# Kernel optimization log

Hardware: AMD Instinct MI355X
Metric: run time of the kernel (lower is better)

The kernel has to match this reference:

```python
import jax, jax.numpy as jnp
import numpy as np

N = 100000  # nodes
E = 1600000  # edges


def gcn_layer(x, src, dst, W, b, n):
    # GCNConv with normalize=True: add self-loops, symmetric deg normalization,
    # linear transform, scatter-add aggregate, add bias, then ReLU (applied by caller).
    loop = jnp.arange(n, dtype=src.dtype)
    s = jnp.concatenate([src, loop])
    d = jnp.concatenate([dst, loop])
    w = jnp.ones(s.shape[0], x.dtype)
    deg = jax.ops.segment_sum(w, d, num_segments=n)
    dis = jnp.where(deg > 0, jax.lax.rsqrt(deg), 0.0)
    norm = dis[s] * w * dis[d]            # [E+N]
    h = x @ W                              # [N, out]
    msg = h[s] * norm[:, None]             # [E+N, out] gather + scale
    out = jax.ops.segment_sum(msg, d, num_segments=n) + b
    return out


def setup_inputs() -> dict:
    key = jax.random.key(0)
    ks = jax.random.split(key, 8)
    d = 128
    sc = 0.05
    return {
        "x": jax.random.normal(ks[0], (N, d), jnp.float32),
        "edge_index": jax.random.randint(ks[1], (2, E), 0, N, jnp.int32),
        "W1": jax.random.normal(ks[2], (d, d), jnp.float32) * sc,
        "b1": jnp.zeros((d,), jnp.float32),
        "W2": jax.random.normal(ks[3], (d, d), jnp.float32) * sc,
        "b2": jnp.zeros((d,), jnp.float32),
        "W3": jax.random.normal(ks[4], (d, d), jnp.float32) * sc,
        "b3": jnp.zeros((d,), jnp.float32),
        "Wm1": jax.random.normal(ks[5], (d, d), jnp.float32) * sc,
        "bm1": jnp.zeros((d,), jnp.float32),
        "Wm2": jax.random.normal(ks[6], (d, 40), jnp.float32) * sc,
        "bm2": jnp.zeros((40,), jnp.float32),
    }


def reference(x, edge_index, W1, b1, W2, b2, W3, b3, Wm1, bm1, Wm2, bm2):
    src, dst = edge_index[0], edge_index[1]
    n = x.shape[0]
    h = x
    for W, b in ((W1, b1), (W2, b2), (W3, b3)):
        h = jax.nn.relu(gcn_layer(h, src, dst, W, b, n))  # emb_normlize=False
    emb = h  # concate=False -> last layer output
    # MLP head: Linear -> ELU -> (dropout p=0, eval) -> Linear -> softmax
    m = jax.nn.elu(emb @ Wm1 + bm1)
    logits = m @ Wm2 + bm2
    probs = jax.nn.softmax(logits, axis=-1)
    return (logits, probs, emb)
```

## Files before the change

### kernel.cpp

```cpp
#include <hip/hip_runtime.h>
#include <math.h>

#define D 128
#define BINW 256
#define MAXBIN 400
#define ACHUNK 4096
#define BCAP 6144
#define SBCAP 8192

typedef __attribute__((ext_vector_type(4))) float floatx4;
typedef __attribute__((ext_vector_type(8))) _Float16 half8;
typedef __attribute__((ext_vector_type(4))) _Float16 half4;


__global__ __launch_bounds__(256) void k_zero(int* __restrict__ p, int n) {
  int i = blockIdx.x * 256 + threadIdx.x;
  if (i < n) p[i] = 0;
}

__global__ __launch_bounds__(256) void k_passA(const int* __restrict__ src,
                                               const int* __restrict__ dst,
                                               int* __restrict__ gbincur,
                                               unsigned* __restrict__ staging,
                                               int E, int nbin) {
  __shared__ int hist[MAXBIN];
  __shared__ int lstart[MAXBIN];
  __shared__ int lcur[MAXBIN];
  __shared__ int runbase[MAXBIN];
  __shared__ int runcnt[MAXBIN];
  __shared__ int sd[256];
  __shared__ unsigned sbuf[ACHUNK];

  int tid = threadIdx.x;
  int e0 = blockIdx.x * ACHUNK;
  int e1 = e0 + ACHUNK < E ? e0 + ACHUNK : E;

  for (int i = tid; i < nbin; i += 256) hist[i] = 0;
  __syncthreads();
  for (int e = e0 + tid; e < e1; e += 256) atomicAdd(&hist[dst[e] >> 8], 1);
  __syncthreads();

  int a = (2 * tid < nbin) ? hist[2 * tid] : 0;
  int b = (2 * tid + 1 < nbin) ? hist[2 * tid + 1] : 0;
  int s = a + b;
  sd[tid] = s;
  __syncthreads();
  for (int off = 1; off < 256; off <<= 1) {
    int t = (tid >= off) ? sd[tid - off] : 0;
    __syncthreads();
    sd[tid] += t;
    __syncthreads();
  }
  int excl = sd[tid] - s;
  if (2 * tid < nbin) lstart[2 * tid] = excl;
  if (2 * tid + 1 < nbin) lstart[2 * tid + 1] = excl + a;
  __syncthreads();

  for (int bx = tid; bx < nbin; bx += 256) {
    int cb = hist[bx];
    int old = cb ? atomicAdd(&gbincur[bx], cb) : 0;
    int lim = SBCAP - old;
    runcnt[bx] = cb < lim ? cb : (lim > 0 ? lim : 0);
    runbase[bx] = bx * SBCAP + old;
    lcur[bx] = lstart[bx];
  }
  __syncthreads();

  for (int e = e0 + tid; e < e1; e += 256) {
    int dd = dst[e];
    int bb = dd >> 8;
    int p = atomicAdd(&lcur[bb], 1);
    sbuf[p] = ((unsigned)src[e] << 8) | (unsigned)(dd & 255);
  }
  __syncthreads();

  int wv = tid >> 6, ln = tid & 63;
  for (int bx = wv; bx < nbin; bx += 4) {
    int cb = runcnt[bx], ls = lstart[bx], rb = runbase[bx];
    for (int i = ln; i < cb; i += 64) staging[rb + i] = sbuf[ls + i];
  }
}

__global__ __launch_bounds__(256) void k_nodehist(const unsigned* __restrict__ staging,
                                                  const int* __restrict__ gbincur,
                                                  int* __restrict__ counts, int N) {
  __shared__ int cnt[BINW];
  int b = blockIdx.x;
  cnt[threadIdx.x] = 0;
  __syncthreads();
  int len = gbincur[b];
  if (len > SBCAP) len = SBCAP;
  int s = b * SBCAP;
  for (int i = (int)threadIdx.x; i < len; i += 256)
    atomicAdd(&cnt[staging[s + i] & 255], 1);
  __syncthreads();
  int node = b * BINW + (int)threadIdx.x;
  if (node < N) counts[node] = cnt[threadIdx.x];
}

__global__ __launch_bounds__(256) void k_scan1(const int* __restrict__ in,
                                               int* __restrict__ out,
                                               int* __restrict__ bsum, int n) {
  __shared__ int sd[256];
  int tid = threadIdx.x;
  int base = blockIdx.x * 1024 + tid * 4;
  int v0 = 0, v1 = 0, v2 = 0, v3 = 0;
  if (base + 3 < n) {
    int4 t = *(const int4*)(in + base);
    v0 = t.x; v1 = t.y; v2 = t.z; v3 = t.w;
  } else {
    if (base     < n) v0 = in[base];
    if (base + 1 < n) v1 = in[base + 1];
    if (base + 2 < n) v2 = in[base + 2];
    if (base + 3 < n) v3 = in[base + 3];
  }
  int s = v0 + v1 + v2 + v3;
  sd[tid] = s;
  __syncthreads();
  for (int off = 1; off < 256; off <<= 1) {
    int t = (tid >= off) ? sd[tid - off] : 0;
    __syncthreads();
    sd[tid] += t;
    __syncthreads();
  }
  int incl = sd[tid];
  int excl = incl - s;
  if (tid == 255) bsum[blockIdx.x] = incl;
  int r = excl;
  if (base     < n) out[base]     = r; r += v0;
  if (base + 1 < n) out[base + 1] = r; r += v1;
  if (base + 2 < n) out[base + 2] = r; r += v2;
  if (base + 3 < n) out[base + 3] = r;
}

__global__ __launch_bounds__(256) void k_scan2(int* __restrict__ bsum, int nb) {
  __shared__ int sd[256];
  int tid = threadIdx.x;
  int v = (tid < nb) ? bsum[tid] : 0;
  sd[tid] = v;
  __syncthreads();
  for (int off = 1; off < 256; off <<= 1) {
    int t = (tid >= off) ? sd[tid - off] : 0;
    __syncthreads();
    sd[tid] += t;
    __syncthreads();
  }
  int excl = sd[tid] - v;
  if (tid < nb) bsum[tid] = excl;
}

__global__ __launch_bounds__(256) void k_finish(int* __restrict__ rowptr,
                                                float* __restrict__ dis,
                                                const int* __restrict__ counts,
                                                const int* __restrict__ bsum, int n) {
  int i = blockIdx.x * 256 + threadIdx.x;
  if (i < n) {
    int r = rowptr[i] + bsum[i >> 10];
    rowptr[i] = r;
    dis[i] = rsqrtf((float)(counts[i] + 1));
  }
}

__global__ __launch_bounds__(256) void k_passB2(const unsigned* __restrict__ staging,
                                                const int* __restrict__ gbincur,
                                                const int* __restrict__ rowptr,
                                                const float* __restrict__ dis,
                                                int2* __restrict__ cpack, int N) {
  __shared__ int lcnt[BINW];
  __shared__ int2 obuf[BCAP];
  int b = blockIdx.x, tid = threadIdx.x;
  int node0 = b * BINW;
  int len = gbincur[b];
  if (len > SBCAP) len = SBCAP;
  int s = b * SBCAP;
  int base = rowptr[node0];
  int node = node0 + tid;
  lcnt[tid] = (node < N) ? (rowptr[node] - base) : 0;
  __syncthreads();
  if (len <= BCAP) {
    for (int i = tid; i < len; i += 256) {
      unsigned pk = staging[s + i];
      int sn = (int)(pk >> 8), dl = (int)(pk & 255u);
      float nw = dis[sn] * dis[node0 + dl];
      int p = atomicAdd(&lcnt[dl], 1);
      obuf[p] = make_int2(sn, __float_as_int(nw));
    }
    __syncthreads();
    for (int i = tid; i < len; i += 256) cpack[base + i] = obuf[i];
  } else {
    for (int i = tid; i < len; i += 256) {
      unsigned pk = staging[s + i];
      int sn = (int)(pk >> 8), dl = (int)(pk & 255u);
      float nw = dis[sn] * dis[node0 + dl];
      int p = atomicAdd(&lcnt[dl], 1);
      cpack[base + p] = make_int2(sn, __float_as_int(nw));
    }
  }
}


__global__ __launch_bounds__(256) void k_prep(const float* __restrict__ W1,
                                              const float* __restrict__ W2,
                                              const float* __restrict__ W3,
                                              const float* __restrict__ Wm1,
                                              const float* __restrict__ Wm2,
                                              _Float16* __restrict__ wsplit,
                                              _Float16* __restrict__ w2h,
                                              _Float16* __restrict__ w2l) {
  int idx = blockIdx.x * 256 + threadIdx.x;
  if (idx < 65536) {
    int w = idx >> 14;
    int rem = idx & 16383;
    int c = rem >> 7, k = rem & 127;
    const float* Ws = (w == 0) ? W1 : (w == 1) ? W2 : (w == 2) ? W3 : Wm1;
    float v = Ws[k * D + c];
    _Float16 hi = (_Float16)v;
    _Float16 lo = (_Float16)(v - (float)hi);
    wsplit[(size_t)w * 32768 + rem] = hi;
    wsplit[(size_t)w * 32768 + 16384 + rem] = lo;
  } else if (idx < 65536 + 6144) {
    int i2 = idx - 65536;
    int c = i2 >> 7, k = i2 & 127;
    float v = (c < 40) ? Wm2[k * 40 + c] : 0.f;
    _Float16 hi = (_Float16)v;
    _Float16 lo = (_Float16)(v - (float)hi);
    w2h[i2] = hi;
    w2l[i2] = lo;
  }
}


__device__ __forceinline__ float elu1(float x) {
  return x > 0.f ? x : (expf(x) - 1.f);
}

template <int AMODE>
__device__ __forceinline__ void loadA(const float* __restrict__ Xf,
                                      const _Float16* __restrict__ Xh,
                                      long rc, int q, half8* ah, half8* al) {
  if (AMODE == 2) {
#pragma unroll
    for (int ks = 0; ks < 4; ks++)
      ah[ks] = *(const half8*)(Xh + rc * D + ks * 32 + q * 8);
  } else {
    const floatx4* x0 = (const floatx4*)(Xf + rc * D);
#pragma unroll
    for (int ks = 0; ks < 4; ks++) {
      floatx4 a0 = x0[ks * 8 + q * 2], a0b = x0[ks * 8 + q * 2 + 1];
#pragma unroll
      for (int j = 0; j < 4; j++) {
        float v = a0[j]; _Float16 h = (_Float16)v;
        ah[ks][j] = h; al[ks][j] = (_Float16)(v - (float)h);
        v = a0b[j]; h = (_Float16)v;
        ah[ks][4 + j] = h; al[ks][4 + j] = (_Float16)(v - (float)h);
      }
    }
  }
}

template <int AMODE, int ACT>
__global__ __launch_bounds__(256, 2) void k_gemm(const float* __restrict__ Xf,
                                                 const _Float16* __restrict__ Xh,
                                                 const _Float16* __restrict__ Whf,
                                                 const _Float16* __restrict__ Wlf,
                                                 const float* __restrict__ bias,
                                                 _Float16* __restrict__ Yh,
                                                 int n, int ntiles) {
  int tid = threadIdx.x;
  int wave = tid >> 6, lane = tid & 63;
  int q = lane >> 4, r = lane & 15;
  int colhalf = wave & 1;
  int stream = wave >> 1;

  half8 wf[4][4][2];
#pragma unroll
  for (int ct = 0; ct < 4; ct++) {
    int c = colhalf * 64 + ct * 16 + r;
#pragma unroll
    for (int ks = 0; ks < 4; ks++) {
      wf[ct][ks][0] = *(const half8*)(Whf + c * D + ks * 32 + q * 8);
      wf[ct][ks][1] = *(const half8*)(Wlf + c * D + ks * 32 + q * 8);
    }
  }

  int tstride = gridDim.x * 2;
  int t = blockIdx.x * 2 + stream;
  if (t >= ntiles) return;

  half8 ah[4], al[4], ahn[4], aln[4];
  {
    long row = (long)t * 16 + r;
    long rc = row < n ? row : (n - 1);
    loadA<AMODE>(Xf, Xh, rc, q, ah, al);
  }

  while (t < ntiles) {
    int tn = t + tstride;
    if (tn < ntiles) {
      long rown = (long)tn * 16 + r;
      long rcn = rown < n ? rown : (n - 1);
      loadA<AMODE>(Xf, Xh, rcn, q, ahn, aln);
    }

    floatx4 acc[4];
#pragma unroll
    for (int ct = 0; ct < 4; ct++) acc[ct] = (floatx4){0.f, 0.f, 0.f, 0.f};
#pragma unroll
    for (int ks = 0; ks < 4; ks++) {
#pragma unroll
      for (int ct = 0; ct < 4; ct++) {
        acc[ct] = __builtin_amdgcn_mfma_f32_16x16x32_f16(wf[ct][ks][0], ah[ks], acc[ct], 0, 0, 0);
        acc[ct] = __builtin_amdgcn_mfma_f32_16x16x32_f16(wf[ct][ks][1], ah[ks], acc[ct], 0, 0, 0);
        if (AMODE == 0)
          acc[ct] = __builtin_amdgcn_mfma_f32_16x16x32_f16(wf[ct][ks][0], al[ks], acc[ct], 0, 0, 0);
      }
    }

    long row = (long)t * 16 + r;
    if (row < n) {
#pragma unroll
      for (int ct = 0; ct < 4; ct++) {
        int c0 = colhalf * 64 + ct * 16 + q * 4;
        floatx4 v = acc[ct];
        if (bias) {
          floatx4 bb = *(const floatx4*)(bias + c0);
#pragma unroll
          for (int i = 0; i < 4; i++) v[i] += bb[i];
        }
        half4 out;
#pragma unroll
        for (int i = 0; i < 4; i++) {
          float vv = v[i];
          if (ACT == 1) vv = elu1(vv);
          out[i] = (_Float16)vv;
        }
        *(half4*)&Yh[row * D + c0] = out;
      }
    }

#pragma unroll
    for (int ks = 0; ks < 4; ks++) { ah[ks] = ahn[ks]; al[ks] = aln[ks]; }
    t = tn;
  }
}


__global__ __launch_bounds__(256) void k_agg(const _Float16* __restrict__ T,
                                             const int* __restrict__ rowptr,
                                             const int* __restrict__ counts,
                                             const int2* __restrict__ cpack,
                                             const float* __restrict__ dis,
                                             const float* __restrict__ bias,
                                             _Float16* __restrict__ Yh,
                                             float* __restrict__ Yf, int n) {
  int tid = threadIdx.x;
  int wave = tid >> 6;
  int lane = tid & 63;
  int g = lane >> 4;
  int r16 = lane & 15;
  int node = blockIdx.x * 16 + wave * 4 + g;
  bool actv = node < n;
  int nodec = actv ? node : 0;

  const half8* T8 = (const half8*)T;

  int s = actv ? rowptr[nodec] : 0;
  int c = actv ? counts[nodec] : 0;
  float dv = actv ? dis[nodec] : 0.f;
  float dv2 = dv * dv;

  half8 t = T8[(size_t)nodec * 16 + r16];
  float acc[8];
#pragma unroll
  for (int k = 0; k < 8; k++) acc[k] = (float)t[k] * dv2;

  int j = 0;
  for (; j + 7 < c; j += 8) {
    int2 m0 = cpack[s + j],     m1 = cpack[s + j + 1];
    int2 m2 = cpack[s + j + 2], m3 = cpack[s + j + 3];
    int2 m4 = cpack[s + j + 4], m5 = cpack[s + j + 5];
    int2 m6 = cpack[s + j + 6], m7 = cpack[s + j + 7];
    half8 v0 = T8[(size_t)m0.x * 16 + r16];
    half8 v1 = T8[(size_t)m1.x * 16 + r16];
    half8 v2 = T8[(size_t)m2.x * 16 + r16];
    half8 v3 = T8[(size_t)m3.x * 16 + r16];
    half8 v4 = T8[(size_t)m4.x * 16 + r16];
    half8 v5 = T8[(size_t)m5.x * 16 + r16];
    half8 v6 = T8[(size_t)m6.x * 16 + r16];
    half8 v7 = T8[(size_t)m7.x * 16 + r16];
    float n0 = __int_as_float(m0.y), n1 = __int_as_float(m1.y);
    float n2 = __int_as_float(m2.y), n3 = __int_as_float(m3.y);
    float n4 = __int_as_float(m4.y), n5 = __int_as_float(m5.y);
    float n6 = __int_as_float(m6.y), n7 = __int_as_float(m7.y);
#pragma unroll
    for (int k = 0; k < 8; k++) {
      acc[k] += (float)v0[k] * n0;
      acc[k] += (float)v1[k] * n1;
      acc[k] += (float)v2[k] * n2;
      acc[k] += (float)v3[k] * n3;
      acc[k] += (float)v4[k] * n4;
      acc[k] += (float)v5[k] * n5;
      acc[k] += (float)v6[k] * n6;
      acc[k] += (float)v7[k] * n7;
    }
  }
  for (; j + 3 < c; j += 4) {
    int2 m0 = cpack[s + j],     m1 = cpack[s + j + 1];
    int2 m2 = cpack[s + j + 2], m3 = cpack[s + j + 3];
    half8 v0 = T8[(size_t)m0.x * 16 + r16];
    half8 v1 = T8[(size_t)m1.x * 16 + r16];
    half8 v2 = T8[(size_t)m2.x * 16 + r16];
    half8 v3 = T8[(size_t)m3.x * 16 + r16];
    float n0 = __int_as_float(m0.y), n1 = __int_as_float(m1.y);
    float n2 = __int_as_float(m2.y), n3 = __int_as_float(m3.y);
#pragma unroll
    for (int k = 0; k < 8; k++) {
      acc[k] += (float)v0[k] * n0;
      acc[k] += (float)v1[k] * n1;
      acc[k] += (float)v2[k] * n2;
      acc[k] += (float)v3[k] * n3;
    }
  }
  for (; j < c; ++j) {
    int2 m = cpack[s + j];
    half8 v = T8[(size_t)m.x * 16 + r16];
    float nw = __int_as_float(m.y);
#pragma unroll
    for (int k = 0; k < 8; k++) acc[k] += (float)v[k] * nw;
  }

  if (actv) {
    const floatx4* b4 = (const floatx4*)(bias + r16 * 8);
    floatx4 bb0 = b4[0], bb1 = b4[1];
    half8 oh;
    float of[8];
#pragma unroll
    for (int k = 0; k < 8; k++) {
      float bv = (k < 4) ? bb0[k] : bb1[k - 4];
      float o = fmaxf(acc[k] + bv, 0.f);
      of[k] = o;
      oh[k] = (_Float16)o;
    }
    *(half8*)&Yh[(size_t)node * D + r16 * 8] = oh;
    if (Yf) {
      floatx4 o0 = {of[0], of[1], of[2], of[3]};
      floatx4 o1 = {of[4], of[5], of[6], of[7]};
      floatx4* yp = (floatx4*)(Yf + (size_t)node * D + r16 * 8);
      yp[0] = o0;
      yp[1] = o1;
    }
  }
}


__global__ __launch_bounds__(256, 2) void k_head(const _Float16* __restrict__ M,
                                                 const _Float16* __restrict__ Whf,
                                                 const _Float16* __restrict__ Wlf,
                                                 const float* __restrict__ b,
                                                 float* __restrict__ logits,
                                                 float* __restrict__ probs,
                                                 int n, int ntiles) {
  int tid = threadIdx.x;
  int wave = tid >> 6, lane = tid & 63;
  int q = lane >> 4, r = lane & 15;

  half8 wf[3][4][2];
#pragma unroll
  for (int ct = 0; ct < 3; ct++) {
    int c = ct * 16 + r;
#pragma unroll
    for (int ks = 0; ks < 4; ks++) {
      wf[ct][ks][0] = *(const half8*)(Whf + c * D + ks * 32 + q * 8);
      wf[ct][ks][1] = *(const half8*)(Wlf + c * D + ks * 32 + q * 8);
    }
  }

  int tstride = gridDim.x * 4;
  for (int t = blockIdx.x * 4 + wave; t < ntiles; t += tstride) {
    long row = (long)t * 16 + r;
    long rc = row < n ? row : (n - 1);
    half8 a[4];
#pragma unroll
    for (int ks = 0; ks < 4; ks++)
      a[ks] = *(const half8*)(M + rc * D + ks * 32 + q * 8);

    floatx4 acc[3];
#pragma unroll
    for (int ct = 0; ct < 3; ct++) acc[ct] = (floatx4){0.f, 0.f, 0.f, 0.f};
#pragma unroll
    for (int ks = 0; ks < 4; ks++) {
#pragma unroll
      for (int ct = 0; ct < 3; ct++) {
        acc[ct] = __builtin_amdgcn_mfma_f32_16x16x32_f16(wf[ct][ks][0], a[ks], acc[ct], 0, 0, 0);
        acc[ct] = __builtin_amdgcn_mfma_f32_16x16x32_f16(wf[ct][ks][1], a[ks], acc[ct], 0, 0, 0);
      }
    }

    float v[3][4];
    float mx = -INFINITY;
#pragma unroll
    for (int ct = 0; ct < 3; ct++) {
      int c0 = ct * 16 + q * 4;
      bool valid = (ct < 2) || (q < 2);
      if (valid) {
        floatx4 bb = *(const floatx4*)(b + c0);
#pragma unroll
        for (int i = 0; i < 4; i++) {
          v[ct][i] = acc[ct][i] + bb[i];
          mx = fmaxf(mx, v[ct][i]);
        }
      } else {
#pragma unroll
        for (int i = 0; i < 4; i++) v[ct][i] = -INFINITY;
      }
    }
    mx = fmaxf(mx, __shfl_xor(mx, 16));
    mx = fmaxf(mx, __shfl_xor(mx, 32));

    float e[3][4];
    float sm = 0.f;
#pragma unroll
    for (int ct = 0; ct < 3; ct++) {
      bool valid = (ct < 2) || (q < 2);
#pragma unroll
      for (int i = 0; i < 4; i++) {
        float ev = valid ? expf(v[ct][i] - mx) : 0.f;
        e[ct][i] = ev;
        sm += ev;
      }
    }
    sm += __shfl_xor(sm, 16);
    sm += __shfl_xor(sm, 32);
    float inv = 1.f / sm;

    if (row < n) {
      float* lp = logits + row * 40;
      float* pp = probs + row * 40;
#pragma unroll
      for (int ct = 0; ct < 3; ct++) {
        int c0 = ct * 16 + q * 4;
        bool valid = (ct < 2) || (q < 2);
        if (valid) {
          floatx4 lv, pv;
#pragma unroll
          for (int i = 0; i < 4; i++) { lv[i] = v[ct][i]; pv[i] = e[ct][i] * inv; }
          *(floatx4*)(lp + c0) = lv;
          *(floatx4*)(pp + c0) = pv;
        }
      }
    }
  }
}


extern "C" void kernel_launch(void* const* d_in, const int* in_sizes, int n_in,
                              void* d_out, int out_size, void* d_ws, size_t ws_size,
                              hipStream_t stream) {
  const float* x   = (const float*)d_in[0];
  const int*   ei  = (const int*)d_in[1];
  const float* W1  = (const float*)d_in[2];
  const float* b1  = (const float*)d_in[3];
  const float* W2  = (const float*)d_in[4];
  const float* b2  = (const float*)d_in[5];
  const float* W3  = (const float*)d_in[6];
  const float* b3  = (const float*)d_in[7];
  const float* Wm1 = (const float*)d_in[8];
  const float* bm1 = (const float*)d_in[9];
  const float* Wm2 = (const float*)d_in[10];
  const float* bm2 = (const float*)d_in[11];

  int N = in_sizes[0] / D;
  int E = in_sizes[1] / 2;
  const int* srcp = ei;
  const int* dstp = ei + E;
  int NBIN = (N + BINW - 1) / BINW;
  int NTILES = (N + 15) / 16;

  char* w = (char*)d_ws;
  auto alloc = [&](size_t bytes) -> char* {
    char* p = w;
    w += (bytes + 255) & ~(size_t)255;
    return p;
  };
  int*   counts = (int*)alloc((size_t)N * 4);
  int*   rowptr = (int*)alloc((size_t)N * 4);
  float* dis    = (float*)alloc((size_t)N * 4);
  int*   bsum   = (int*)alloc(1024);
  int*   gbincur= (int*)alloc(MAXBIN * 4);
  _Float16* wsplit = (_Float16*)alloc(4 * 32768 * 2);
  _Float16* w2h    = (_Float16*)alloc(6144 * 2);
  _Float16* w2l    = (_Float16*)alloc(6144 * 2);
  int2*  cpack  = (int2*)alloc((size_t)E * 8);
  _Float16* tmp_h  = (_Float16*)alloc((size_t)N * D * 2);
  _Float16* hbuf_h = (_Float16*)alloc((size_t)N * D * 2);
  unsigned* staging = (unsigned*)tmp_h;

  float* logits = (float*)d_out;
  float* probs  = logits + (size_t)N * 40;
  float* emb    = probs + (size_t)N * 40;

  k_prep<<<(65536 + 6144 + 255) / 256, 256, 0, stream>>>(W1, W2, W3, Wm1, Wm2,
                                                         wsplit, w2h, w2l);
  k_zero<<<(NBIN + 255) / 256, 256, 0, stream>>>(gbincur, NBIN);
  k_passA<<<(E + ACHUNK - 1) / ACHUNK, 256, 0, stream>>>(srcp, dstp, gbincur,
                                                         staging, E, NBIN);
  k_nodehist<<<NBIN, 256, 0, stream>>>(staging, gbincur, counts, N);
  int nb = (N + 1023) / 1024;
  k_scan1<<<nb, 256, 0, stream>>>(counts, rowptr, bsum, N);
  k_scan2<<<1, 256, 0, stream>>>(bsum, nb);
  k_finish<<<(N + 255) / 256, 256, 0, stream>>>(rowptr, dis, counts, bsum, N);
  k_passB2<<<NBIN, 256, 0, stream>>>(staging, gbincur, rowptr, dis, cpack, N);

  int gblocks = 512;
  int ablocks = (N + 15) / 16;
  const _Float16* Whf1 = wsplit;
  const _Float16* Wlf1 = wsplit + 16384;
  const _Float16* Whf2 = wsplit + 32768;
  const _Float16* Wlf2 = wsplit + 32768 + 16384;
  const _Float16* Whf3 = wsplit + 2 * 32768;
  const _Float16* Wlf3 = wsplit + 2 * 32768 + 16384;
  const _Float16* Whm1 = wsplit + 3 * 32768;
  const _Float16* Wlm1 = wsplit + 3 * 32768 + 16384;

  k_gemm<0, 0><<<gblocks, 256, 0, stream>>>(x, nullptr, Whf1, Wlf1, nullptr,
                                            tmp_h, N, NTILES);
  k_agg<<<ablocks, 256, 0, stream>>>(tmp_h, rowptr, counts, cpack, dis, b1,
                                     hbuf_h, nullptr, N);
  k_gemm<2, 0><<<gblocks, 256, 0, stream>>>(nullptr, hbuf_h, Whf2, Wlf2, nullptr,
                                            tmp_h, N, NTILES);
  k_agg<<<ablocks, 256, 0, stream>>>(tmp_h, rowptr, counts, cpack, dis, b2,
                                     hbuf_h, nullptr, N);
  k_gemm<2, 0><<<gblocks, 256, 0, stream>>>(nullptr, hbuf_h, Whf3, Wlf3, nullptr,
                                            tmp_h, N, NTILES);
  k_agg<<<ablocks, 256, 0, stream>>>(tmp_h, rowptr, counts, cpack, dis, b3,
                                     hbuf_h, emb, N);
  k_gemm<2, 1><<<gblocks, 256, 0, stream>>>(nullptr, hbuf_h, Whm1, Wlm1, bm1,
                                            tmp_h, N, NTILES);
  k_head<<<gblocks, 256, 0, stream>>>(tmp_h, w2h, w2l, bm2,
                                      logits, probs, N, NTILES);
}
```

Before: 512.4 us.

## Fuse first GEMM, edge binning pass, and weight prep into one heterogeneous launch

Merges the layer-1 GEMM (which now splits W1 into fp16 hi/lo in registers instead of reading preprocessed weights), the edge bucketing pass A, and the remaining weight-split prep into a single kernel whose blocks take different roles by block index. The staging buffer moves to hbuf_h so the GEMM can write tmp_h concurrently, and the gbincur zeroing kernel becomes a memset. The aim is to remove launch gaps and let independent compute-bound and memory-bound work overlap. The cost is larger shared memory and register use per block in one kernel, and GEMM blocks that each reload W1 from global memory.

```diff
diff --git a/kernel.cpp b/kernel.cpp
--- a/kernel.cpp
+++ b/kernel.cpp
@@ -12,74 +12,6 @@
 typedef __attribute__((ext_vector_type(8))) _Float16 half8;
 typedef __attribute__((ext_vector_type(4))) _Float16 half4;
 
-
-__global__ __launch_bounds__(256) void k_zero(int* __restrict__ p, int n) {
-  int i = blockIdx.x * 256 + threadIdx.x;
-  if (i < n) p[i] = 0;
-}
-
-__global__ __launch_bounds__(256) void k_passA(const int* __restrict__ src,
-                                               const int* __restrict__ dst,
-                                               int* __restrict__ gbincur,
-                                               unsigned* __restrict__ staging,
-                                               int E, int nbin) {
-  __shared__ int hist[MAXBIN];
-  __shared__ int lstart[MAXBIN];
-  __shared__ int lcur[MAXBIN];
-  __shared__ int runbase[MAXBIN];
-  __shared__ int runcnt[MAXBIN];
-  __shared__ int sd[256];
-  __shared__ unsigned sbuf[ACHUNK];
-
-  int tid = threadIdx.x;
-  int e0 = blockIdx.x * ACHUNK;
-  int e1 = e0 + ACHUNK < E ? e0 + ACHUNK : E;
-
-  for (int i = tid; i < nbin; i += 256) hist[i] = 0;
-  __syncthreads();
-  for (int e = e0 + tid; e < e1; e += 256) atomicAdd(&hist[dst[e] >> 8], 1);
-  __syncthreads();
-
-  int a = (2 * tid < nbin) ? hist[2 * tid] : 0;
-  int b = (2 * tid + 1 < nbin) ? hist[2 * tid + 1] : 0;
-  int s = a + b;
-  sd[tid] = s;
-  __syncthreads();
-  for (int off = 1; off < 256; off <<= 1) {
-    int t = (tid >= off) ? sd[tid - off] : 0;
-    __syncthreads();
-    sd[tid] += t;
-    __syncthreads();
-  }
-  int excl = sd[tid] - s;
-  if (2 * tid < nbin) lstart[2 * tid] = excl;
-  if (2 * tid + 1 < nbin) lstart[2 * tid + 1] = excl + a;
-  __syncthreads();
-
-  for (int bx = tid; bx < nbin; bx += 256) {
-    int cb = hist[bx];
-    int old = cb ? atomicAdd(&gbincur[bx], cb) : 0;
-    int lim = SBCAP - old;
-    runcnt[bx] = cb < lim ? cb : (lim > 0 ? lim : 0);
-    runbase[bx] = bx * SBCAP + old;
-    lcur[bx] = lstart[bx];
-  }
-  __syncthreads();
-
-  for (int e = e0 + tid; e < e1; e += 256) {
-    int dd = dst[e];
-    int bb = dd >> 8;
-    int p = atomicAdd(&lcur[bb], 1);
-    sbuf[p] = ((unsigned)src[e] << 8) | (unsigned)(dd & 255);
-  }
-  __syncthreads();
-
-  int wv = tid >> 6, ln = tid & 63;
-  for (int bx = wv; bx < nbin; bx += 4) {
-    int cb = runcnt[bx], ls = lstart[bx], rb = runbase[bx];
-    for (int i = ln; i < cb; i += 64) staging[rb + i] = sbuf[ls + i];
-  }
-}
 
 __global__ __launch_bounds__(256) void k_nodehist(const unsigned* __restrict__ staging,
                                                   const int* __restrict__ gbincur,
@@ -199,40 +131,197 @@
 }
 
 
-__global__ __launch_bounds__(256) void k_prep(const float* __restrict__ W1,
-                                              const float* __restrict__ W2,
-                                              const float* __restrict__ W3,
-                                              const float* __restrict__ Wm1,
-                                              const float* __restrict__ Wm2,
-                                              _Float16* __restrict__ wsplit,
-                                              _Float16* __restrict__ w2h,
-                                              _Float16* __restrict__ w2l) {
-  int idx = blockIdx.x * 256 + threadIdx.x;
-  if (idx < 65536) {
-    int w = idx >> 14;
-    int rem = idx & 16383;
-    int c = rem >> 7, k = rem & 127;
-    const float* Ws = (w == 0) ? W1 : (w == 1) ? W2 : (w == 2) ? W3 : Wm1;
-    float v = Ws[k * D + c];
-    _Float16 hi = (_Float16)v;
-    _Float16 lo = (_Float16)(v - (float)hi);
-    wsplit[(size_t)w * 32768 + rem] = hi;
-    wsplit[(size_t)w * 32768 + 16384 + rem] = lo;
-  } else if (idx < 65536 + 6144) {
-    int i2 = idx - 65536;
-    int c = i2 >> 7, k = i2 & 127;
-    float v = (c < 40) ? Wm2[k * 40 + c] : 0.f;
-    _Float16 hi = (_Float16)v;
-    _Float16 lo = (_Float16)(v - (float)hi);
-    w2h[i2] = hi;
-    w2l[i2] = lo;
-  }
-}
-
-
 __device__ __forceinline__ float elu1(float x) {
   return x > 0.f ? x : (expf(x) - 1.f);
 }
+
+__global__ __launch_bounds__(256, 2) void k_front(
+    const float* __restrict__ x, const float* __restrict__ W1g,
+    _Float16* __restrict__ Yh, int n, int ntiles, int gb1,
+    const int* __restrict__ src, const int* __restrict__ dst,
+    int* __restrict__ gbincur, unsigned* __restrict__ staging, int E, int nbin,
+    int pab,
+    const float* __restrict__ W2, const float* __restrict__ W3,
+    const float* __restrict__ Wm1, const float* __restrict__ Wm2,
+    _Float16* __restrict__ wsplit, _Float16* __restrict__ w2h,
+    _Float16* __restrict__ w2l) {
+  __shared__ int hist[MAXBIN];
+  __shared__ int lstart[MAXBIN];
+  __shared__ int lcur[MAXBIN];
+  __shared__ int runbase[MAXBIN];
+  __shared__ int runcnt[MAXBIN];
+  __shared__ int sd[256];
+  __shared__ unsigned sbuf[ACHUNK];
+
+  int tid = threadIdx.x;
+  int bid = blockIdx.x;
+
+  if (bid < gb1) {
+    int wave = tid >> 6, lane = tid & 63;
+    int q = lane >> 4, r = lane & 15;
+    int colhalf = wave & 1;
+    int stream = wave >> 1;
+
+    half8 wf[4][4][2];
+#pragma unroll
+    for (int ct = 0; ct < 4; ct++) {
+      int c = colhalf * 64 + ct * 16 + r;
+#pragma unroll
+      for (int ks = 0; ks < 4; ks++) {
+#pragma unroll
+        for (int j = 0; j < 8; j++) {
+          float v = W1g[(ks * 32 + q * 8 + j) * D + c];
+          _Float16 h = (_Float16)v;
+          wf[ct][ks][0][j] = h;
+          wf[ct][ks][1][j] = (_Float16)(v - (float)h);
+        }
+      }
+    }
+
+    int tstride = gb1 * 2;
+    int t = bid * 2 + stream;
+    if (t >= ntiles) return;
+
+    half8 ah[4], al[4], ahn[4], aln[4];
+    {
+      long row = (long)t * 16 + r;
+      long rc = row < n ? row : (n - 1);
+      const floatx4* x0 = (const floatx4*)(x + rc * D);
+#pragma unroll
+      for (int ks = 0; ks < 4; ks++) {
+        floatx4 a0 = x0[ks * 8 + q * 2], a0b = x0[ks * 8 + q * 2 + 1];
+#pragma unroll
+        for (int j = 0; j < 4; j++) {
+          float v = a0[j]; _Float16 h = (_Float16)v;
+          ah[ks][j] = h; al[ks][j] = (_Float16)(v - (float)h);
+          v = a0b[j]; h = (_Float16)v;
+          ah[ks][4 + j] = h; al[ks][4 + j] = (_Float16)(v - (float)h);
+        }
+      }
+    }
+
+    while (t < ntiles) {
+      int tn = t + tstride;
+      if (tn < ntiles) {
+        long rown = (long)tn * 16 + r;
+        long rcn = rown < n ? rown : (n - 1);
+        const floatx4* x0 = (const floatx4*)(x + rcn * D);
+#pragma unroll
+        for (int ks = 0; ks < 4; ks++) {
+          floatx4 a0 = x0[ks * 8 + q * 2], a0b = x0[ks * 8 + q * 2 + 1];
+#pragma unroll
+          for (int j = 0; j < 4; j++) {
+            float v = a0[j]; _Float16 h = (_Float16)v;
+            ahn[ks][j] = h; aln[ks][j] = (_Float16)(v - (float)h);
+            v = a0b[j]; h = (_Float16)v;
+            ahn[ks][4 + j] = h; aln[ks][4 + j] = (_Float16)(v - (float)h);
+          }
+        }
+      }
+
+      floatx4 acc[4];
+#pragma unroll
+      for (int ct = 0; ct < 4; ct++) acc[ct] = (floatx4){0.f, 0.f, 0.f, 0.f};
+#pragma unroll
+      for (int ks = 0; ks < 4; ks++) {
+#pragma unroll
+        for (int ct = 0; ct < 4; ct++) {
+          acc[ct] = __builtin_amdgcn_mfma_f32_16x16x32_f16(wf[ct][ks][0], ah[ks], acc[ct], 0, 0, 0);
+          acc[ct] = __builtin_amdgcn_mfma_f32_16x16x32_f16(wf[ct][ks][1], ah[ks], acc[ct], 0, 0, 0);
+          acc[ct] = __builtin_amdgcn_mfma_f32_16x16x32_f16(wf[ct][ks][0], al[ks], acc[ct], 0, 0, 0);
+        }
+      }
+
+      long row = (long)t * 16 + r;
+      if (row < n) {
+#pragma unroll
+        for (int ct = 0; ct < 4; ct++) {
+          int c0 = colhalf * 64 + ct * 16 + q * 4;
+          floatx4 v = acc[ct];
+          half4 out;
+#pragma unroll
+          for (int i = 0; i < 4; i++) out[i] = (_Float16)v[i];
+          *(half4*)&Yh[row * D + c0] = out;
+        }
+      }
+
+#pragma unroll
+      for (int ks = 0; ks < 4; ks++) { ah[ks] = ahn[ks]; al[ks] = aln[ks]; }
+      t = tn;
+    }
+  } else if (bid < gb1 + pab) {
+    int cb_ = bid - gb1;
+    int e0 = cb_ * ACHUNK;
+    int e1 = e0 + ACHUNK < E ? e0 + ACHUNK : E;
+
+    for (int i = tid; i < nbin; i += 256) hist[i] = 0;
+    __syncthreads();
+    for (int e = e0 + tid; e < e1; e += 256) atomicAdd(&hist[dst[e] >> 8], 1);
+    __syncthreads();
+
+    int a = (2 * tid < nbin) ? hist[2 * tid] : 0;
+    int b = (2 * tid + 1 < nbin) ? hist[2 * tid + 1] : 0;
+    int s = a + b;
+    sd[tid] = s;
+    __syncthreads();
+    for (int off = 1; off < 256; off <<= 1) {
+      int t2 = (tid >= off) ? sd[tid - off] : 0;
+      __syncthreads();
+      sd[tid] += t2;
+      __syncthreads();
+    }
+    int excl = sd[tid] - s;
+    if (2 * tid < nbin) lstart[2 * tid] = excl;
+    if (2 * tid + 1 < nbin) lstart[2 * tid + 1] = excl + a;
+    __syncthreads();
+
+    for (int bx = tid; bx < nbin; bx += 256) {
+      int cb = hist[bx];
+      int old = cb ? atomicAdd(&gbincur[bx], cb) : 0;
+      int lim = SBCAP - old;
+      runcnt[bx] = cb < lim ? cb : (lim > 0 ? lim : 0);
+      runbase[bx] = bx * SBCAP + old;
+      lcur[bx] = lstart[bx];
+    }
+    __syncthreads();
+
+    for (int e = e0 + tid; e < e1; e += 256) {
+      int dd = dst[e];
+      int bb = dd >> 8;
+      int p = atomicAdd(&lcur[bb], 1);
+      sbuf[p] = ((unsigned)src[e] << 8) | (unsigned)(dd & 255);
+    }
+    __syncthreads();
+
+    int wv = tid >> 6, ln = tid & 63;
+    for (int bx = wv; bx < nbin; bx += 4) {
+      int cb = runcnt[bx], ls = lstart[bx], rb = runbase[bx];
+      for (int i = ln; i < cb; i += 64) staging[rb + i] = sbuf[ls + i];
+    }
+  } else {
+    int idx = (bid - gb1 - pab) * 256 + tid;
+    if (idx < 49152) {
+      int w = idx >> 14;
+      int rem = idx & 16383;
+      int c = rem >> 7, k = rem & 127;
+      const float* Ws = (w == 0) ? W2 : (w == 1) ? W3 : Wm1;
+      float v = Ws[k * D + c];
+      _Float16 hi = (_Float16)v;
+      _Float16 lo = (_Float16)(v - (float)hi);
+      wsplit[(size_t)(w + 1) * 32768 + rem] = hi;
+      wsplit[(size_t)(w + 1) * 32768 + 16384 + rem] = lo;
+    } else if (idx < 49152 + 6144) {
+      int i2 = idx - 49152;
+      int c = i2 >> 7, k = i2 & 127;
+      float v = (c < 40) ? Wm2[k * 40 + c] : 0.f;
+      _Float16 hi = (_Float16)v;
+      _Float16 lo = (_Float16)(v - (float)hi);
+      w2h[i2] = hi;
+      w2l[i2] = lo;
+    }
+  }
+}
+
 
 template <int AMODE>
 __device__ __forceinline__ void loadA(const float* __restrict__ Xf,
@@ -593,17 +682,22 @@
   int2*  cpack  = (int2*)alloc((size_t)E * 8);
   _Float16* tmp_h  = (_Float16*)alloc((size_t)N * D * 2);
   _Float16* hbuf_h = (_Float16*)alloc((size_t)N * D * 2);
-  unsigned* staging = (unsigned*)tmp_h;
+  unsigned* staging = (unsigned*)hbuf_h;
 
   float* logits = (float*)d_out;
   float* probs  = logits + (size_t)N * 40;
   float* emb    = probs + (size_t)N * 40;
 
-  k_prep<<<(65536 + 6144 + 255) / 256, 256, 0, stream>>>(W1, W2, W3, Wm1, Wm2,
-                                                         wsplit, w2h, w2l);
-  k_zero<<<(NBIN + 255) / 256, 256, 0, stream>>>(gbincur, NBIN);
-  k_passA<<<(E + ACHUNK - 1) / ACHUNK, 256, 0, stream>>>(srcp, dstp, gbincur,
-                                                         staging, E, NBIN);
+  hipMemsetAsync(gbincur, 0, (size_t)NBIN * 4, stream);
+
+  int GB1 = 256;
+  int PAB = (E + ACHUNK - 1) / ACHUNK;
+  int PREPB = (49152 + 6144 + 255) / 256;
+  k_front<<<GB1 + PAB + PREPB, 256, 0, stream>>>(
+      x, W1, tmp_h, N, NTILES, GB1,
+      srcp, dstp, gbincur, staging, E, NBIN, PAB,
+      W2, W3, Wm1, Wm2, wsplit, w2h, w2l);
+
   k_nodehist<<<NBIN, 256, 0, stream>>>(staging, gbincur, counts, N);
   int nb = (N + 1023) / 1024;
   k_scan1<<<nb, 256, 0, stream>>>(counts, rowptr, bsum, N);
@@ -613,8 +707,6 @@
 
   int gblocks = 512;
   int ablocks = (N + 15) / 16;
-  const _Float16* Whf1 = wsplit;
-  const _Float16* Wlf1 = wsplit + 16384;
   const _Float16* Whf2 = wsplit + 32768;
   const _Float16* Wlf2 = wsplit + 32768 + 16384;
   const _Float16* Whf3 = wsplit + 2 * 32768;
@@ -622,8 +714,6 @@
   const _Float16* Whm1 = wsplit + 3 * 32768;
   const _Float16* Wlm1 = wsplit + 3 * 32768 + 16384;
 
-  k_gemm<0, 0><<<gblocks, 256, 0, stream>>>(x, nullptr, Whf1, Wlf1, nullptr,
-                                            tmp_h, N, NTILES);
   k_agg<<<ablocks, 256, 0, stream>>>(tmp_h, rowptr, counts, cpack, dis, b1,
                                      hbuf_h, nullptr, N);
   k_gemm<2, 0><<<gblocks, 256, 0, stream>>>(nullptr, hbuf_h, Whf2, Wlf2, nullptr,
```

Result: faster. 500.6 us (-2.3%).
